# Performance work log

Hardware: AMD Instinct MI355X
Metric: run time of the kernel (lower is better)

The kernel has to match this reference:

```python
import jax, jax.numpy as jnp
import numpy as np

# Qwen3-Next GatedDeltaNet dims (tp_size = 1)
H = 2048          # hidden_size
HK, HV = 16, 32   # num_k_heads, num_v_heads
G = HV // HK      # v-heads per k-head
DK, DV = 128, 128 # head_k_dim, head_v_dim
KEY_DIM = HK * DK        # 2048
VAL_DIM = HV * DV        # 4096
CONV_DIM = 2 * KEY_DIM + VAL_DIM   # 8192
QKVZ = 2 * KEY_DIM + 2 * VAL_DIM   # 12288
BA = 2 * HV
K = 4             # conv kernel size
L = 4096          # tokens (one prefill sequence)
EPS = 1e-6


def setup_inputs() -> dict:
    key = jax.random.key(0)
    ks = jax.random.split(key, 5)
    s = lambda k, shape, sc: jax.random.normal(k, shape, jnp.float32) * sc
    return {
        'hidden_states': s(ks[0], (L, H), 1.0),
        'in_proj_w': s(ks[1], (H, QKVZ + BA), H ** -0.5),
        'conv_w': s(ks[2], (CONV_DIM, K), 0.25),
        'A_log': jnp.zeros((HV,), jnp.float32),
        'dt_bias': jnp.ones((HV,), jnp.float32),
        'norm_w': jnp.ones((DV,), jnp.float32),
        'out_proj_w': s(ks[3], (VAL_DIM, H), VAL_DIM ** -0.5),
    }


def _l2norm(x):
    return x * jax.lax.rsqrt(jnp.sum(x * x, axis=-1, keepdims=True) + EPS)


def _gdn_forward(hidden_states, in_proj_w, conv_w, A_log, dt_bias, norm_w, out_proj_w):
    # in_proj -> split qkvz / ba, fix_query_key_value_ordering
    proj = hidden_states @ in_proj_w                       # [L, QKVZ+BA]
    qkvz, ba = proj[:, :QKVZ], proj[:, QKVZ:]
    qkvz = qkvz.reshape(L, HK, 2 * DK + 2 * G * DV)        # per-k-head layout
    q = qkvz[:, :, :DK]                                    # [L,HK,DK]
    k = qkvz[:, :, DK:2 * DK]                              # [L,HK,DK]
    v = qkvz[:, :, 2 * DK:2 * DK + G * DV].reshape(L, HV, DV)
    z = qkvz[:, :, 2 * DK + G * DV:].reshape(L, HV, DV)
    ba = ba.reshape(L, HK, 2 * G)
    b = ba[:, :, :G].reshape(L, HV)
    a = ba[:, :, G:].reshape(L, HV)

    # depthwise causal conv1d over time (kernel K, left pad K-1) + silu
    mixed_qkv = jnp.concatenate(
        [q.reshape(L, KEY_DIM), k.reshape(L, KEY_DIM), v.reshape(L, VAL_DIM)], axis=-1)
    xp = jnp.pad(mixed_qkv, ((K - 1, 0), (0, 0)))
    conv_out = sum(conv_w[:, j] * xp[j:j + L] for j in range(K))
    mixed_qkv = jax.nn.silu(conv_out)

    q = mixed_qkv[:, :KEY_DIM].reshape(L, HK, DK)
    k = mixed_qkv[:, KEY_DIM:2 * KEY_DIM].reshape(L, HK, DK)
    v = mixed_qkv[:, 2 * KEY_DIM:].reshape(L, HV, DV)

    # gating: beta = sigmoid(b); g = -exp(A_log) * softplus(a + dt_bias)
    beta = jax.nn.sigmoid(b)                               # [L,HV]
    g = -jnp.exp(A_log) * jax.nn.softplus(a + dt_bias)     # [L,HV] (log decay)

    # expand k-heads to v-heads, qk l2-norm, scale q
    q = jnp.repeat(q, G, axis=1)                           # [L,HV,DK]
    k = jnp.repeat(k, G, axis=1)
    q = _l2norm(q) * (DK ** -0.5)
    k = _l2norm(k)

    # gated delta rule recurrence over time (state S: [HV, DK, DV])
    def step(S, inp):
        q_t, k_t, v_t, g_t, b_t = inp
        S = S * jnp.exp(g_t)[:, None, None]
        delta = (v_t - jnp.einsum('hk,hkv->hv', k_t, S)) * b_t[:, None]
        S = S + jnp.einsum('hk,hv->hkv', k_t, delta)
        o = jnp.einsum('hk,hkv->hv', q_t, S)
        return S, o

    S0 = jnp.zeros((HV, DK, DV), jnp.float32)
    _, core = jax.lax.scan(step, S0, (q, k, v, g, beta))   # core: [L,HV,DV]

    # gated RMSNorm (norm before gate): RMSNorm(x)*w*silu(z)
    var = jnp.mean(core * core, axis=-1, keepdims=True)
    core = core * jax.lax.rsqrt(var + EPS) * norm_w
    core = core * jax.nn.silu(z)

    return core.reshape(L, VAL_DIM) @ out_proj_w           # [L, H]


def reference(hidden_states, in_proj_w, conv_w, A_log, dt_bias, norm_w, out_proj_w):
    return _gdn_forward(hidden_states, in_proj_w, conv_w, A_log, dt_bias, norm_w, out_proj_w)
```

## Files before the change

kernel.cpp:

```cpp
#include <hip/hip_runtime.h>
#include <hip/hip_bf16.h>

#define L_SEQ 4096
#define HDIM 2048
#define NPROJA 8256
#define NPACK 12352
#define WLD 12352
#define EPS_ 1e-6f

using bf16 = __hip_bfloat16;
typedef __attribute__((ext_vector_type(8))) short short8;
typedef __attribute__((ext_vector_type(4))) float f32x4;

__device__ __forceinline__ float b2f(bf16 x) { return __bfloat162float(x); }
__device__ __forceinline__ bf16 f2b(float x) { return __float2bfloat16(x); }
__device__ __forceinline__ unsigned short b2u(bf16 x) {
  union { bf16 b; unsigned short u; } c; c.b = x; return c.u;
}
__device__ __forceinline__ void* swz(void* base, int row, int rowbytes, int colbyte) {
  return (void*)((char*)base + row * rowbytes + (colbyte ^ ((row & 7) << 4)));
}
__device__ __forceinline__ const void* swzc(const void* base, int row, int rowbytes, int colbyte) {
  return (const void*)((const char*)base + row * rowbytes + (colbyte ^ ((row & 7) << 4)));
}
__device__ __forceinline__ void* swzk(void* base, int row, int colbyte) {
  return (void*)((char*)base + row * 128 + (colbyte ^ (((row >> 3) & 7) << 4)));
}
__device__ __forceinline__ const void* swzkc(const void* base, int row, int colbyte) {
  return (const void*)((const char*)base + row * 128 + (colbyte ^ (((row >> 3) & 7) << 4)));
}

__device__ __forceinline__ void async_copy16(const void* g, void* l) {
  __builtin_amdgcn_global_load_lds(
      (const __attribute__((address_space(1))) void*)g,
      (__attribute__((address_space(3))) void*)l, 16, 0, 0);
}

__global__ __launch_bounds__(256) void cvt_bf16(const float* __restrict__ in,
                                                bf16* __restrict__ outp) {
  int i = (blockIdx.x * 256 + threadIdx.x) * 4;
  float4 v = *(const float4*)&in[i];
  bf16 o4[4] = {f2b(v.x), f2b(v.y), f2b(v.z), f2b(v.w)};
  *(ushort4*)&outp[i] = *(ushort4*)o4;
}

template <int MODE>
__device__ __forceinline__ int pmap(int n) {
  if constexpr (MODE == 3) {
    if (n < 2048) return (n >> 7) * 768 + (n & 127);
    else if (n < 4096) { int m = n - 2048; return (m >> 7) * 768 + 128 + (m & 127); }
    else if (n < 8192) { int m = n - 4096; return (m >> 8) * 768 + 256 + (m & 255); }
    else if (n < 8256) return 12288 + (n - 8192);
    else { int m = n - 8256; return (m >> 8) * 768 + 512 + (m & 255); }
  } else {
    return n;
  }
}

template <int MODE>
__global__ __launch_bounds__(256) void transpose_w(
    const float* __restrict__ W, bf16* __restrict__ Bt, int ldw, int Kd) {
  __shared__ float T[64][65];
  const int nb = blockIdx.x * 64, kb = blockIdx.y * 64;
  const int tid = threadIdx.x;
  const int c = tid & 63, gq = tid >> 6;
  const int sbase = pmap<MODE>(nb);
#pragma unroll
  for (int i = 0; i < 16; ++i) {
    int r = gq * 16 + i;
    T[c][r] = W[(size_t)(kb + r) * ldw + sbase + c];
  }
  __syncthreads();
#pragma unroll
  for (int i = 0; i < 16; ++i) {
    int n = gq * 16 + i;
    Bt[(size_t)(nb + n) * Kd + kb + c] = f2b(T[n][c]);
  }
}

template <int ROUTE>
__global__ __launch_bounds__(256) void gemm_bt(
    const bf16* __restrict__ A, const bf16* __restrict__ Bt,
    void* __restrict__ Cp, bf16* __restrict__ Cz, int N, int Kd,
    int MBnum, int NBnum) {
  __shared__ bf16 As[2][128 * 32];
  __shared__ bf16 Bs[2][128 * 32];
  const int tid = threadIdx.x;
  const int wave = tid >> 6, lane = tid & 63;
  const int l15 = lane & 15, quad = lane >> 4;

  int m_blk, n_blk;
  {
    const int CW = 32;
    int fullc = NBnum / CW;
    int rem = NBnum - fullc * CW;
    int thr = fullc * CW * MBnum;
    int wg = blockIdx.x;
    if (wg < thr) {
      int cw = CW * MBnum;
      int chunk = wg / cw, w = wg - chunk * cw;
      n_blk = chunk * CW + (w & (CW - 1));
      m_blk = w / CW;
    } else {
      int w2 = wg - thr;
      int r = rem ? rem : 1;
      n_blk = fullc * CW + w2 % r;
      m_blk = w2 / r;
    }
  }
  const int m0 = m_blk * 128, n0 = n_blk * 128;
  const int mw = (wave >> 1) * 64, nw = (wave & 1) * 64;

  f32x4 acc[4][4];
#pragma unroll
  for (int i = 0; i < 4; i++)
#pragma unroll
    for (int j = 0; j < 4; j++) acc[i][j] = {0.f, 0.f, 0.f, 0.f};

  const bf16* a_src0 = A + (size_t)(m0 + (tid >> 2)) * Kd + (tid & 3) * 8;
  const bf16* a_src1 = a_src0 + (size_t)64 * Kd;
  const bf16* b_src0 = Bt + (size_t)(n0 + (tid >> 2)) * Kd + (tid & 3) * 8;
  const bf16* b_src1 = b_src0 + (size_t)64 * Kd;
  const int d0 = tid * 8, d1 = (tid + 256) * 8;

  async_copy16(a_src0, &As[0][d0]);
  async_copy16(a_src1, &As[0][d1]);
  async_copy16(b_src0, &Bs[0][d0]);
  async_copy16(b_src1, &Bs[0][d1]);

  int cur = 0;
  for (int k0 = 0; k0 < Kd; k0 += 32, cur ^= 1) {
    __syncthreads();
    if (k0 + 32 < Kd) {
      const int nk = k0 + 32, nb = cur ^ 1;
      async_copy16(a_src0 + nk, &As[nb][d0]);
      async_copy16(a_src1 + nk, &As[nb][d1]);
      async_copy16(b_src0 + nk, &Bs[nb][d0]);
      async_copy16(b_src1 + nk, &Bs[nb][d1]);
    }
    short8 af[4], bfr[4];
#pragma unroll
    for (int i = 0; i < 4; i++)
      af[i] = *(const short8*)&As[cur][(mw + i * 16 + l15) * 32 + quad * 8];
#pragma unroll
    for (int j = 0; j < 4; j++)
      bfr[j] = *(const short8*)&Bs[cur][(nw + j * 16 + l15) * 32 + quad * 8];
#pragma unroll
    for (int i = 0; i < 4; i++)
#pragma unroll
      for (int j = 0; j < 4; j++)
        acc[i][j] = __builtin_amdgcn_mfma_f32_16x16x32_bf16(af[i], bfr[j],
                                                            acc[i][j], 0, 0, 0);
  }

#pragma unroll
  for (int i = 0; i < 4; i++) {
#pragma unroll
    for (int j = 0; j < 4; j++) {
      int col = n0 + nw + j * 16 + l15;
      if (col < N) {
#pragma unroll
        for (int r = 0; r < 4; r++) {
          int row = m0 + mw + i * 16 + quad * 4 + r;
          if (ROUTE == 0) {
            ((float*)Cp)[(size_t)row * N + col] = acc[i][j][r];
          } else {
            if (col < NPROJA)
              ((bf16*)Cp)[(size_t)row * NPROJA + col] = f2b(acc[i][j][r]);
            else
              Cz[(size_t)row * 4096 + (col - NPROJA)] = f2b(acc[i][j][r]);
          }
        }
      }
    }
  }
}

__global__ __launch_bounds__(128) void conv_norm_qk(
    const bf16* __restrict__ proj, const float* __restrict__ conv_w,
    bf16* __restrict__ qn, bf16* __restrict__ kn) {
  const int t = blockIdx.x >> 4, hk = blockIdx.x & 15;
  const int d = threadIdx.x;
  const int cq = hk * 128 + d;
  const int ck = 2048 + hk * 128 + d;
  float sq = 0.f, sk = 0.f;
#pragma unroll
  for (int j = 0; j < 4; j++) {
    int ts = t + j - 3;
    if (ts >= 0) {
      sq += conv_w[cq * 4 + j] * b2f(proj[(size_t)ts * NPROJA + cq]);
      sk += conv_w[ck * 4 + j] * b2f(proj[(size_t)ts * NPROJA + ck]);
    }
  }
  float qv = sq / (1.f + expf(-sq));
  float kv = sk / (1.f + expf(-sk));
  float ssq = qv * qv, ssk = kv * kv;
#pragma unroll
  for (int off = 32; off > 0; off >>= 1) {
    ssq += __shfl_down(ssq, off, 64);
    ssk += __shfl_down(ssk, off, 64);
  }
  __shared__ float red[4];
  if ((d & 63) == 0) {
    red[(d >> 6) * 2] = ssq;
    red[(d >> 6) * 2 + 1] = ssk;
  }
  __syncthreads();
  float sumq = red[0] + red[2];
  float sumk = red[1] + red[3];
  size_t o = (size_t)(t * 16 + hk) * 128 + d;
  qn[o] = f2b(qv * rsqrtf(sumq + EPS_) * 0.08838834764831845f);
  kn[o] = f2b(kv * rsqrtf(sumk + EPS_));
}

__global__ __launch_bounds__(256) void conv_silu_v(
    const bf16* __restrict__ proj, const float* __restrict__ conv_w,
    bf16* __restrict__ vbuf) {
  int idx = blockIdx.x * 256 + threadIdx.x;
  int t = idx >> 12, c = idx & 4095;
  int chan = 4096 + c;
  float s = 0.f;
#pragma unroll
  for (int j = 0; j < 4; j++) {
    int ts = t + j - 3;
    if (ts >= 0) s += conv_w[chan * 4 + j] * b2f(proj[(size_t)ts * NPROJA + chan]);
  }
  vbuf[idx] = f2b(s / (1.f + expf(-s)));
}

__global__ __launch_bounds__(256) void compute_bg(
    const bf16* __restrict__ proj, const float* __restrict__ A_log,
    const float* __restrict__ dt_bias, float* __restrict__ beta_arr,
    float* __restrict__ g_arr) {
  int idx = blockIdx.x * 256 + threadIdx.x;
  int t = idx >> 5, hv = idx & 31;
  size_t base = (size_t)t * NPROJA + 8192 + (hv >> 1) * 4 + (hv & 1);
  float b = b2f(proj[base]);
  float a = b2f(proj[base + 2]);
  beta_arr[idx] = 1.f / (1.f + expf(-b));
  float x = a + dt_bias[hv];
  float sp = (x > 20.f) ? x : log1pf(expf(x));
  g_arr[idx] = -expf(A_log[hv]) * sp;
}

__global__ __launch_bounds__(512) void precompute_chunk(
    const bf16* __restrict__ kn, const bf16* __restrict__ vbuf,
    const float* __restrict__ g_arr, const float* __restrict__ beta_arr,
    bf16* __restrict__ TV, bf16* __restrict__ TK) {
  const int c = blockIdx.x >> 5, h = blockIdx.x & 31, hk = h >> 1;
  const int t0 = c * 64, tid = threadIdx.x;
  const int wave = tid >> 6, lane = tid & 63, l15 = lane & 15, quad = lane >> 4;
  __shared__ bf16 Ks[64 * 128];
  __shared__ float X[64][256];
  __shared__ float BA[64][65];
  __shared__ float cgs[64], bet[64], eKs[64];

  {
    const int row = tid >> 4, s = tid & 15;
    short8 v0 = *(const short8*)(kn + ((size_t)(t0 + row) * 16 + hk) * 128 + s * 8);
    short8 v1 = *(const short8*)(kn + ((size_t)(t0 + 32 + row) * 16 + hk) * 128 + s * 8);
    *(short8*)swz(Ks, row, 256, s * 16) = v0;
    *(short8*)swz(Ks, row + 32, 256, s * 16) = v1;
  }
  if (tid < 64) {
    float bb = beta_arr[(size_t)(t0 + tid) * 32 + h];
    bet[tid] = bb;
    float x = g_arr[(size_t)(t0 + tid) * 32 + h];
#pragma unroll
    for (int off = 1; off < 64; off <<= 1) {
      float o = __shfl_up(x, off, 64);
      if (tid >= off) x += o;
    }
    cgs[tid] = x;
    eKs[tid] = bb * expf(x);
  }
  __syncthreads();

#pragma unroll
  for (int s = 0; s < 2; ++s) {
    const int b = wave * 2 + s, bi = b >> 2, bj = b & 3;
    if (bi >= bj) {
      f32x4 acc = {0.f, 0.f, 0.f, 0.f};
      const int ar = bi * 16 + l15, br = bj * 16 + l15;
#pragma unroll
      for (int ks = 0; ks < 4; ++ks) {
        const int cb = ks * 64 + quad * 16;
        short8 af = *(const short8*)swzc(Ks, ar, 256, cb);
        short8 bf = *(const short8*)swzc(Ks, br, 256, cb);
        acc = __builtin_amdgcn_mfma_f32_16x16x32_bf16(af, bf, acc, 0, 0, 0);
      }
#pragma unroll
      for (int r = 0; r < 4; ++r) {
        const int i = bi * 16 + quad * 4 + r, j = bj * 16 + l15;
        if (j < i) BA[i][j] = bet[i] * expf(cgs[i] - cgs[j]) * acc[r];
      }
    }
  }
  {
    const int i = tid >> 4, s = tid & 15;
#pragma unroll
    for (int half = 0; half < 2; ++half) {
      const int row = i + half * 32;
      short8 vv = *(const short8*)(vbuf + (size_t)(t0 + row) * 4096 + h * 128 + s * 8);
      short8 kv = *(const short8*)swzc(Ks, row, 256, s * 16);
      bf16 tv_[8], tk_[8];
      *(short8*)tv_ = vv;
      *(short8*)tk_ = kv;
      const float bb = bet[row], ee = eKs[row];
      float o0[8], o1[8];
#pragma unroll
      for (int k = 0; k < 8; ++k) {
        o0[k] = bb * b2f(tv_[k]);
        o1[k] = ee * b2f(tk_[k]);
      }
      *(float4*)&X[row][s * 8] = *(float4*)&o0[0];
      *(float4*)&X[row][s * 8 + 4] = *(float4*)&o0[4];
      *(float4*)&X[row][128 + s * 8] = *(float4*)&o1[0];
      *(float4*)&X[row][128 + s * 8 + 4] = *(float4*)&o1[4];
    }
  }

  const int li = tid >> 5, g4 = (tid & 31) * 4;
#pragma unroll
  for (int t = 0; t < 4; ++t) {
    const int i0 = t * 16;
    __syncthreads();
    if (t > 0) {
      const int gi = i0 + li;
      float4 a0 = *(float4*)&X[gi][g4];
      float4 a1 = *(float4*)&X[gi][128 + g4];
      for (int j = 0; j < i0; ++j) {
        const float bij = BA[gi][j];
        float4 x0 = *(float4*)&X[j][g4];
        float4 x1 = *(float4*)&X[j][128 + g4];
        a0.x -= bij * x0.x; a0.y -= bij * x0.y;
        a0.z -= bij * x0.z; a0.w -= bij * x0.w;
        a1.x -= bij * x1.x; a1.y -= bij * x1.y;
        a1.z -= bij * x1.z; a1.w -= bij * x1.w;
      }
      *(float4*)&X[gi][g4] = a0;
      *(float4*)&X[gi][128 + g4] = a1;
      __syncthreads();
    }
    if (tid < 256) {
      const int d = tid;
#pragma unroll
      for (int i2 = 1; i2 < 16; ++i2) {
        const int i = i0 + i2;
        float s = 0.f;
        for (int j = i0; j < i; ++j) s += BA[i][j] * X[j][d];
        X[i][d] -= s;
      }
    }
  }
  __syncthreads();
  for (int e = tid; e < 8192; e += 512) {
    int i = e >> 7, d = e & 127;
    size_t o = ((size_t)(t0 + i) * 32 + h) * 128 + d;
    TV[o] = f2b(X[i][d]);
    TK[o] = f2b(X[i][128 + d]);
  }
}

__global__ __launch_bounds__(512) void seq_kernel(
    bf16* TVU,
    const bf16* __restrict__ TKg, const bf16* __restrict__ qn,
    const bf16* __restrict__ kn, const float* __restrict__ g_arr,
    bf16* __restrict__ Oin) {
  const int h = blockIdx.x >> 1, dvh = blockIdx.x & 1, hk = h >> 1;
  const int dv0 = dvh * 64;
  const int tid = threadIdx.x;
  const int wave = tid >> 6, lane = tid & 63, l15 = lane & 15, quad = lane >> 4;
  const int mi = wave >> 1, half = wave & 1;
  const int srow = tid >> 4, scol = tid & 15;

  __shared__ bf16 STh[64 * 128], STl[64 * 128];
  __shared__ bf16 UTh[64 * 64], UTl[64 * 64];
  __shared__ bf16 TKs[64 * 128];
  __shared__ bf16 Qts[64 * 128];
  __shared__ bf16 KhT[128 * 64];

  for (int e = tid; e < 4096; e += 512) {
    ((unsigned int*)STh)[e] = 0u;
    ((unsigned int*)STl)[e] = 0u;
  }
  f32x4 Sf[4];
#pragma unroll
  for (int i = 0; i < 4; i++) Sf[i] = {0.f, 0.f, 0.f, 0.f};

  short8 tkr0, tkr1, qr0, qr1, kr0, kr1;
  float gv;
  auto issue_loads = [&](int c) {
    const size_t t0 = (size_t)c << 6;
    tkr0 = *(const short8*)(TKg + ((t0 + srow) * 32 + h) * 128 + scol * 8);
    tkr1 = *(const short8*)(TKg + ((t0 + 32 + srow) * 32 + h) * 128 + scol * 8);
    qr0 = *(const short8*)(qn + ((t0 + srow) * 16 + hk) * 128 + scol * 8);
    qr1 = *(const short8*)(qn + ((t0 + 32 + srow) * 16 + hk) * 128 + scol * 8);
    kr0 = *(const short8*)(kn + ((t0 + srow) * 16 + hk) * 128 + scol * 8);
    kr1 = *(const short8*)(kn + ((t0 + 32 + srow) * 16 + hk) * 128 + scol * 8);
    gv = g_arr[(t0 + lane) * 32 + h];
  };
  issue_loads(0);

  for (int c = 0; c < 64; ++c) {
    const int t0 = c << 6;
    __syncthreads();

    bf16 tvp[2][4];
#pragma unroll
    for (int nj = 0; nj < 2; nj++) {
      const int nrow = half * 32 + nj * 16 + l15;
#pragma unroll
      for (int r = 0; r < 4; r++) {
        const int i = mi * 16 + quad * 4 + r;
        tvp[nj][r] = TVU[((size_t)(t0 + i) * 32 + h) * 128 + dv0 + nrow];
      }
    }
    float cg = gv;
#pragma unroll
    for (int off = 1; off < 64; off <<= 1) {
      float o = __shfl_up(cg, off, 64);
      if (lane >= off) cg += o;
    }
    const float cg63 = __shfl(cg, 63, 64);
    const float lam = expf(cg63);
    const float fq = expf(cg);
    const float fk = expf(cg63 - cg);
    *(short8*)swz(TKs, srow, 256, scol * 16) = tkr0;
    *(short8*)swz(TKs, srow + 32, 256, scol * 16) = tkr1;
    {
      const float f0 = __shfl(fq, srow, 64);
      const float f1 = __shfl(fq, srow + 32, 64);
      bf16 ta[8], tb[8];
      *(short8*)ta = qr0;
      *(short8*)tb = qr1;
#pragma unroll
      for (int k = 0; k < 8; k++) {
        ta[k] = f2b(b2f(ta[k]) * f0);
        tb[k] = f2b(b2f(tb[k]) * f1);
      }
      *(short8*)swz(Qts, srow, 256, scol * 16) = *(short8*)ta;
      *(short8*)swz(Qts, srow + 32, 256, scol * 16) = *(short8*)tb;
    }
    {
      const float f0 = __shfl(fk, srow, 64);
      const float f1 = __shfl(fk, srow + 32, 64);
      bf16 ka[8], kb[8];
      *(short8*)ka = kr0;
      *(short8*)kb = kr1;
#pragma unroll
      for (int k = 0; k < 8; k++) {
        const int dk = scol * 8 + k;
        *(bf16*)swzk(KhT, dk, srow * 2) = f2b(b2f(ka[k]) * f0);
        *(bf16*)swzk(KhT, dk, (srow + 32) * 2) = f2b(b2f(kb[k]) * f1);
      }
    }
    issue_loads(c + 1 < 64 ? c + 1 : 63);
    __syncthreads();

    f32x4 oacc[2], xacc[2];
#pragma unroll
    for (int nj = 0; nj < 2; nj++) { oacc[nj] = {0.f,0.f,0.f,0.f}; xacc[nj] = {0.f,0.f,0.f,0.f}; }
    const int arow = mi * 16 + l15;
#pragma unroll
    for (int ks = 0; ks < 4; ++ks) {
      const int cb = ks * 64 + quad * 16;
      short8 aq = *(const short8*)swzc(Qts, arow, 256, cb);
      short8 at = *(const short8*)swzc(TKs, arow, 256, cb);
#pragma unroll
      for (int nj = 0; nj < 2; nj++) {
        const int nrow = half * 32 + nj * 16 + l15;
        short8 bh = *(const short8*)swzc(STh, nrow, 256, cb);
        short8 bl = *(const short8*)swzc(STl, nrow, 256, cb);
        oacc[nj] = __builtin_amdgcn_mfma_f32_16x16x32_bf16(aq, bh, oacc[nj], 0, 0, 0);
        xacc[nj] = __builtin_amdgcn_mfma_f32_16x16x32_bf16(at, bh, xacc[nj], 0, 0, 0);
        xacc[nj] = __builtin_amdgcn_mfma_f32_16x16x32_bf16(at, bl, xacc[nj], 0, 0, 0);
      }
    }
    const int krow = wave * 16 + l15;
    short8 ak0 = *(const short8*)swzkc(KhT, krow, 0 * 64 + quad * 16);
    short8 ak1 = *(const short8*)swzkc(KhT, krow, 1 * 64 + quad * 16);

#pragma unroll
    for (int nj = 0; nj < 2; nj++) {
      const int nrow = half * 32 + nj * 16 + l15;
      unsigned short ph[4], pl[4];
#pragma unroll
      for (int r = 0; r < 4; ++r) {
        const int i = mi * 16 + quad * 4 + r;
        const size_t go = ((size_t)(t0 + i) * 32 + h) * 128 + dv0 + nrow;
        Oin[go] = f2b(oacc[nj][r]);
        float uv = b2f(tvp[nj][r]) - xacc[nj][r];
        bf16 hb = f2b(uv);
        TVU[go] = hb;
        ph[r] = b2u(hb);
        pl[r] = b2u(f2b(uv - b2f(hb)));
      }
      const int cb = (mi * 16 + quad * 4) * 2;
      ushort4 vh; vh.x = ph[0]; vh.y = ph[1]; vh.z = ph[2]; vh.w = ph[3];
      ushort4 vl; vl.x = pl[0]; vl.y = pl[1]; vl.z = pl[2]; vl.w = pl[3];
      *(ushort4*)swz(UTh, nrow, 128, cb) = vh;
      *(ushort4*)swz(UTl, nrow, 128, cb) = vl;
    }
    __syncthreads();

#pragma unroll
    for (int nj = 0; nj < 4; nj++) {
      Sf[nj][0] *= lam; Sf[nj][1] *= lam; Sf[nj][2] *= lam; Sf[nj][3] *= lam;
    }
#pragma unroll
    for (int ks = 0; ks < 2; ++ks) {
      const short8 ak = ks ? ak1 : ak0;
      const int cb = ks * 64 + quad * 16;
#pragma unroll
      for (int nj = 0; nj < 4; nj++) {
        const int nrow = nj * 16 + l15;
        short8 bh = *(const short8*)swzc(UTh, nrow, 128, cb);
        short8 bl = *(const short8*)swzc(UTl, nrow, 128, cb);
        Sf[nj] = __builtin_amdgcn_mfma_f32_16x16x32_bf16(ak, bh, Sf[nj], 0, 0, 0);
        Sf[nj] = __builtin_amdgcn_mfma_f32_16x16x32_bf16(ak, bl, Sf[nj], 0, 0, 0);
      }
    }
#pragma unroll
    for (int nj = 0; nj < 4; nj++) {
      const int nrow = nj * 16 + l15;
      unsigned short ph[4], pl[4];
#pragma unroll
      for (int r = 0; r < 4; ++r) {
        float s = Sf[nj][r];
        bf16 hb = f2b(s);
        ph[r] = b2u(hb);
        pl[r] = b2u(f2b(s - b2f(hb)));
      }
      const int cb = (wave * 16 + quad * 4) * 2;
      ushort4 vh; vh.x = ph[0]; vh.y = ph[1]; vh.z = ph[2]; vh.w = ph[3];
      ushort4 vl; vl.x = pl[0]; vl.y = pl[1]; vl.z = pl[2]; vl.w = pl[3];
      *(ushort4*)swz(STh, nrow, 256, cb) = vh;
      *(ushort4*)swz(STl, nrow, 256, cb) = vl;
    }
  }
}

__global__ __launch_bounds__(512) void pass2_kernel(
    bf16* UC,
    const bf16* __restrict__ Oin, const bf16* __restrict__ qn,
    const bf16* __restrict__ kn, const float* __restrict__ g_arr,
    const bf16* __restrict__ zbuf, const float* __restrict__ norm_w) {
  const int c = blockIdx.x >> 5, h = blockIdx.x & 31, hk = h >> 1;
  const int t0 = c * 64, tid = threadIdx.x;
  __shared__ float Qf[64][129], Kf[64][129];
  __shared__ float Uf[64][128];
  __shared__ float Of[64][129];
  __shared__ float At[64][65];
  __shared__ float cgs[64], nw[128];

  for (int e = tid; e < 1024; e += 512) {
    int row = e >> 4, s = e & 15;
    size_t qko = ((size_t)(t0 + row) * 16 + hk) * 128 + s * 8;
    size_t uo = ((size_t)(t0 + row) * 32 + h) * 128 + s * 8;
    short8 vq = *(const short8*)(qn + qko);
    short8 vk = *(const short8*)(kn + qko);
    short8 vu = *(const short8*)(UC + uo);
    short8 vo = *(const short8*)(Oin + uo);
    bf16 tq[8], tk[8], tu[8], to[8];
    *(short8*)tq = vq; *(short8*)tk = vk; *(short8*)tu = vu; *(short8*)to = vo;
#pragma unroll
    for (int k = 0; k < 8; ++k) {
      Qf[row][s * 8 + k] = b2f(tq[k]);
      Kf[row][s * 8 + k] = b2f(tk[k]);
      Uf[row][s * 8 + k] = b2f(tu[k]);
      Of[row][s * 8 + k] = b2f(to[k]);
    }
  }
  if (tid < 64) {
    float x = g_arr[(size_t)(t0 + tid) * 32 + h];
#pragma unroll
    for (int off = 1; off < 64; off <<= 1) {
      float o = __shfl_up(x, off, 64);
      if (tid >= off) x += o;
    }
    cgs[tid] = x;
  }
  if (tid < 128) nw[tid] = norm_w[tid];
  __syncthreads();
  {
    const int ti = tid >> 4, tj = tid & 15;
    float acc[2][4];
#pragma unroll
    for (int r = 0; r < 2; ++r)
#pragma unroll
      for (int s = 0; s < 4; ++s) acc[r][s] = 0.f;
    for (int dk = 0; dk < 128; ++dk) {
      float a0 = Qf[ti * 2 + 0][dk], a1 = Qf[ti * 2 + 1][dk];
      float c0 = Kf[tj * 4 + 0][dk], c1 = Kf[tj * 4 + 1][dk];
      float c2 = Kf[tj * 4 + 2][dk], c3 = Kf[tj * 4 + 3][dk];
      acc[0][0] += a0 * c0; acc[0][1] += a0 * c1; acc[0][2] += a0 * c2; acc[0][3] += a0 * c3;
      acc[1][0] += a1 * c0; acc[1][1] += a1 * c1; acc[1][2] += a1 * c2; acc[1][3] += a1 * c3;
    }
#pragma unroll
    for (int r = 0; r < 2; ++r)
#pragma unroll
      for (int s = 0; s < 4; ++s) {
        int i = ti * 2 + r, j = tj * 4 + s;
        At[i][j] = (j <= i) ? expf(cgs[i] - cgs[j]) * acc[r][s] : 0.f;
      }
  }
  __syncthreads();
  {
    const int ri = tid >> 4, tn = tid & 15;
    float acc[2][8];
#pragma unroll
    for (int r = 0; r < 2; ++r)
#pragma unroll
      for (int k = 0; k < 8; ++k) acc[r][k] = 0.f;
    for (int j = 0; j < 64; ++j) {
      float a0 = At[ri * 2 + 0][j], a1 = At[ri * 2 + 1][j];
#pragma unroll
      for (int k = 0; k < 8; ++k) {
        float u = Uf[j][tn + 16 * k];
        acc[0][k] += a0 * u;
        acc[1][k] += a1 * u;
      }
    }
#pragma unroll
    for (int r = 0; r < 2; ++r)
#pragma unroll
      for (int k = 0; k < 8; ++k)
        Of[ri * 2 + r][tn + 16 * k] += acc[r][k];
  }
  __syncthreads();
  {
    const int r = tid >> 3, q8 = tid & 7;
    float ss = 0.f;
#pragma unroll
    for (int k = 0; k < 16; ++k) {
      float v = Of[r][q8 + 8 * k];
      ss += v * v;
    }
    ss += __shfl_xor(ss, 1, 64);
    ss += __shfl_xor(ss, 2, 64);
    ss += __shfl_xor(ss, 4, 64);
    float scale = rsqrtf(ss * (1.f / 128.f) + EPS_);
#pragma unroll
    for (int k = 0; k < 16; ++k) {
      int n = q8 + 8 * k;
      float val = Of[r][n] * scale * nw[n];
      float zz = b2f(zbuf[(size_t)(t0 + r) * 4096 + h * 128 + n]);
      val *= zz / (1.f + expf(-zz));
      UC[((size_t)(t0 + r) * 32 + h) * 128 + n] = f2b(val);
    }
  }
}

extern "C" void kernel_launch(void* const* d_in, const int* in_sizes, int n_in,
                              void* d_out, int out_size, void* d_ws,
                              size_t ws_size, hipStream_t stream) {
  const float* hidden = (const float*)d_in[0];
  const float* in_w = (const float*)d_in[1];
  const float* conv_w = (const float*)d_in[2];
  const float* A_log = (const float*)d_in[3];
  const float* dt_bias = (const float*)d_in[4];
  const float* norm_w = (const float*)d_in[5];
  const float* out_w = (const float*)d_in[6];
  float* out = (float*)d_out;

  char* p = (char*)d_ws;
  bf16* projA = (bf16*)p;
  bf16* TV = (bf16*)p;
  bf16* TK = (bf16*)(p + 33554432ULL);
  bf16* zbuf = (bf16*)(p + 67633152ULL);
  char* pR = p + 101187584ULL;
  bf16* vbuf = (bf16*)pR;
  float* beta = (float*)(pR + 33554432ULL);
  float* g = (float*)(pR + 34078720ULL);
  bf16* qn = (bf16*)(pR + 34603008ULL);
  bf16* kn = (bf16*)(pR + 51380224ULL);
  bf16* Bt_in = (bf16*)pR;
  bf16* hb16 = (bf16*)(pR + 50659328ULL);
  bf16* Bt_out = (bf16*)zbuf;

  cvt_bf16<<<(L_SEQ * HDIM) / 1024, 256, 0, stream>>>(hidden, hb16);
  transpose_w<3><<<dim3(193, 32), 256, 0, stream>>>(in_w, Bt_in, WLD, HDIM);
  gemm_bt<1><<<97 * 32, 256, 0, stream>>>(hb16, Bt_in, projA, zbuf,
                                          NPACK, HDIM, 32, 97);
  conv_norm_qk<<<L_SEQ * 16, 128, 0, stream>>>(projA, conv_w, qn, kn);
  conv_silu_v<<<(L_SEQ * 4096) / 256, 256, 0, stream>>>(projA, conv_w, vbuf);
  compute_bg<<<(L_SEQ * 32) / 256, 256, 0, stream>>>(projA, A_log, dt_bias,
                                                     beta, g);
  precompute_chunk<<<2048, 512, 0, stream>>>(kn, vbuf, g, beta, TV, TK);
  seq_kernel<<<64, 512, 0, stream>>>(TV, TK, qn, kn, g, vbuf);
  pass2_kernel<<<2048, 512, 0, stream>>>(TV, vbuf, qn, kn, g, zbuf, norm_w);
  transpose_w<0><<<dim3(32, 64), 256, 0, stream>>>(out_w, Bt_out, 2048, 4096);
  gemm_bt<0><<<16 * 32, 256, 0, stream>>>(TV, Bt_out, out, nullptr,
                                          2048, 4096, 32, 16);
}
```

Before: 1.170 ms.

## Triple-buffer GEMM LDS pipeline and vectorize conv kernels to 8 channels per thread

The bf16 GEMM moves from double to triple buffering. Each k-step waits with vmcnt(4), so one tile load stays in flight while MFMAs run, and there is a single barrier per step. Separately, the conv+silu+l2norm kernel for q/k and the conv+silu kernel for v now give each thread 8 channels, using 16-byte loads and stores, float4 conv weights and a 16-lane xor-shuffle reduction instead of shared memory. This cuts launch count, memory transactions and sync overhead in the elementwise stages, at the cost of more LDS per GEMM block (which may lower occupancy) and more registers per thread.

```diff
diff --git a/kernel.cpp b/kernel.cpp
--- a/kernel.cpp
+++ b/kernel.cpp
@@ -83,8 +83,8 @@
     const bf16* __restrict__ A, const bf16* __restrict__ Bt,
     void* __restrict__ Cp, bf16* __restrict__ Cz, int N, int Kd,
     int MBnum, int NBnum) {
-  __shared__ bf16 As[2][128 * 32];
-  __shared__ bf16 Bs[2][128 * 32];
+  __shared__ bf16 As[3][128 * 32];
+  __shared__ bf16 Bs[3][128 * 32];
   const int tid = threadIdx.x;
   const int wave = tid >> 6, lane = tid & 63;
   const int l15 = lane & 15, quad = lane >> 4;
@@ -127,31 +127,47 @@
   async_copy16(a_src1, &As[0][d1]);
   async_copy16(b_src0, &Bs[0][d0]);
   async_copy16(b_src1, &Bs[0][d1]);
+  async_copy16(a_src0 + 32, &As[1][d0]);
+  async_copy16(a_src1 + 32, &As[1][d1]);
+  async_copy16(b_src0 + 32, &Bs[1][d0]);
+  async_copy16(b_src1 + 32, &Bs[1][d1]);
+
+  auto mfma_step = [&](int bsel) {
+    short8 af[4], bfr[4];
+#pragma unroll
+    for (int i = 0; i < 4; i++)
+      af[i] = *(const short8*)&As[bsel][(mw + i * 16 + l15) * 32 + quad * 8];
+#pragma unroll
+    for (int j = 0; j < 4; j++)
+      bfr[j] = *(const short8*)&Bs[bsel][(nw + j * 16 + l15) * 32 + quad * 8];
+#pragma unroll
+    for (int i = 0; i < 4; i++)
+#pragma unroll
+      for (int j = 0; j < 4; j++)
+        acc[i][j] = __builtin_amdgcn_mfma_f32_16x16x32_bf16(af[i], bfr[j],
+                                                            acc[i][j], 0, 0, 0);
+  };
 
   int cur = 0;
-  for (int k0 = 0; k0 < Kd; k0 += 32, cur ^= 1) {
-    __syncthreads();
-    if (k0 + 32 < Kd) {
-      const int nk = k0 + 32, nb = cur ^ 1;
+  for (int k0 = 0; k0 < Kd - 32; k0 += 32) {
+    asm volatile("s_waitcnt vmcnt(4)" ::: "memory");
+    __builtin_amdgcn_s_barrier();
+    __builtin_amdgcn_sched_barrier(0);
+    const int nk = k0 + 64;
+    if (nk < Kd) {
+      int nb = cur + 2; if (nb >= 3) nb -= 3;
       async_copy16(a_src0 + nk, &As[nb][d0]);
       async_copy16(a_src1 + nk, &As[nb][d1]);
       async_copy16(b_src0 + nk, &Bs[nb][d0]);
       async_copy16(b_src1 + nk, &Bs[nb][d1]);
     }
-    short8 af[4], bfr[4];
-#pragma unroll
-    for (int i = 0; i < 4; i++)
-      af[i] = *(const short8*)&As[cur][(mw + i * 16 + l15) * 32 + quad * 8];
-#pragma unroll
-    for (int j = 0; j < 4; j++)
-      bfr[j] = *(const short8*)&Bs[cur][(nw + j * 16 + l15) * 32 + quad * 8];
-#pragma unroll
-    for (int i = 0; i < 4; i++)
-#pragma unroll
-      for (int j = 0; j < 4; j++)
-        acc[i][j] = __builtin_amdgcn_mfma_f32_16x16x32_bf16(af[i], bfr[j],
-                                                            acc[i][j], 0, 0, 0);
-  }
+    mfma_step(cur);
+    cur = (cur + 1 == 3) ? 0 : cur + 1;
+  }
+  asm volatile("s_waitcnt vmcnt(0)" ::: "memory");
+  __builtin_amdgcn_s_barrier();
+  __builtin_amdgcn_sched_barrier(0);
+  mfma_step(cur);
 
 #pragma unroll
   for (int i = 0; i < 4; i++) {
@@ -179,53 +195,90 @@
 __global__ __launch_bounds__(128) void conv_norm_qk(
     const bf16* __restrict__ proj, const float* __restrict__ conv_w,
     bf16* __restrict__ qn, bf16* __restrict__ kn) {
-  const int t = blockIdx.x >> 4, hk = blockIdx.x & 15;
-  const int d = threadIdx.x;
-  const int cq = hk * 128 + d;
-  const int ck = 2048 + hk * 128 + d;
-  float sq = 0.f, sk = 0.f;
+  const int t = blockIdx.x >> 1, g = blockIdx.x & 1;
+  const int r = threadIdx.x >> 4, s = threadIdx.x & 15;
+  const int hk = g * 8 + r;
+  const int cq = hk * 128 + s * 8;
+  const int ck = 2048 + cq;
+  float4 cwq[8], cwk[8];
+#pragma unroll
+  for (int e = 0; e < 8; ++e) {
+    cwq[e] = *(const float4*)&conv_w[(cq + e) * 4];
+    cwk[e] = *(const float4*)&conv_w[(ck + e) * 4];
+  }
+  float aq[8], ak[8];
+#pragma unroll
+  for (int e = 0; e < 8; ++e) { aq[e] = 0.f; ak[e] = 0.f; }
 #pragma unroll
   for (int j = 0; j < 4; j++) {
     int ts = t + j - 3;
     if (ts >= 0) {
-      sq += conv_w[cq * 4 + j] * b2f(proj[(size_t)ts * NPROJA + cq]);
-      sk += conv_w[ck * 4 + j] * b2f(proj[(size_t)ts * NPROJA + ck]);
-    }
-  }
-  float qv = sq / (1.f + expf(-sq));
-  float kv = sk / (1.f + expf(-sk));
-  float ssq = qv * qv, ssk = kv * kv;
-#pragma unroll
-  for (int off = 32; off > 0; off >>= 1) {
-    ssq += __shfl_down(ssq, off, 64);
-    ssk += __shfl_down(ssk, off, 64);
-  }
-  __shared__ float red[4];
-  if ((d & 63) == 0) {
-    red[(d >> 6) * 2] = ssq;
-    red[(d >> 6) * 2 + 1] = ssk;
-  }
-  __syncthreads();
-  float sumq = red[0] + red[2];
-  float sumk = red[1] + red[3];
-  size_t o = (size_t)(t * 16 + hk) * 128 + d;
-  qn[o] = f2b(qv * rsqrtf(sumq + EPS_) * 0.08838834764831845f);
-  kn[o] = f2b(kv * rsqrtf(sumk + EPS_));
+      short8 vq = *(const short8*)(proj + (size_t)ts * NPROJA + cq);
+      short8 vk = *(const short8*)(proj + (size_t)ts * NPROJA + ck);
+      bf16 tq[8], tk[8];
+      *(short8*)tq = vq;
+      *(short8*)tk = vk;
+#pragma unroll
+      for (int e = 0; e < 8; ++e) {
+        aq[e] += ((const float*)&cwq[e])[j] * b2f(tq[e]);
+        ak[e] += ((const float*)&cwk[e])[j] * b2f(tk[e]);
+      }
+    }
+  }
+  float fq[8], fk[8], ssq = 0.f, ssk = 0.f;
+#pragma unroll
+  for (int e = 0; e < 8; ++e) {
+    fq[e] = aq[e] / (1.f + expf(-aq[e]));
+    fk[e] = ak[e] / (1.f + expf(-ak[e]));
+    ssq += fq[e] * fq[e];
+    ssk += fk[e] * fk[e];
+  }
+#pragma unroll
+  for (int off = 1; off < 16; off <<= 1) {
+    ssq += __shfl_xor(ssq, off, 64);
+    ssk += __shfl_xor(ssk, off, 64);
+  }
+  const float rq = rsqrtf(ssq + EPS_) * 0.08838834764831845f;
+  const float rk = rsqrtf(ssk + EPS_);
+  bf16 wq[8], wk[8];
+#pragma unroll
+  for (int e = 0; e < 8; ++e) {
+    wq[e] = f2b(fq[e] * rq);
+    wk[e] = f2b(fk[e] * rk);
+  }
+  size_t o = (size_t)(t * 16 + hk) * 128 + s * 8;
+  *(short8*)(qn + o) = *(short8*)wq;
+  *(short8*)(kn + o) = *(short8*)wk;
 }
 
 __global__ __launch_bounds__(256) void conv_silu_v(
     const bf16* __restrict__ proj, const float* __restrict__ conv_w,
     bf16* __restrict__ vbuf) {
   int idx = blockIdx.x * 256 + threadIdx.x;
-  int t = idx >> 12, c = idx & 4095;
-  int chan = 4096 + c;
-  float s = 0.f;
+  int t = idx >> 9, c8 = (idx & 511) * 8;
+  int chan = 4096 + c8;
+  float4 cw[8];
+#pragma unroll
+  for (int e = 0; e < 8; ++e) cw[e] = *(const float4*)&conv_w[(chan + e) * 4];
+  float acc[8];
+#pragma unroll
+  for (int e = 0; e < 8; ++e) acc[e] = 0.f;
 #pragma unroll
   for (int j = 0; j < 4; j++) {
     int ts = t + j - 3;
-    if (ts >= 0) s += conv_w[chan * 4 + j] * b2f(proj[(size_t)ts * NPROJA + chan]);
-  }
-  vbuf[idx] = f2b(s / (1.f + expf(-s)));
+    if (ts >= 0) {
+      short8 v = *(const short8*)(proj + (size_t)ts * NPROJA + chan);
+      bf16 tv[8];
+      *(short8*)tv = v;
+#pragma unroll
+      for (int e = 0; e < 8; ++e)
+        acc[e] += ((const float*)&cw[e])[j] * b2f(tv[e]);
+    }
+  }
+  bf16 o[8];
+#pragma unroll
+  for (int e = 0; e < 8; ++e) o[e] = f2b(acc[e] / (1.f + expf(-acc[e])));
+  *(short8*)(vbuf + (size_t)t * 4096 + c8) = *(short8*)o;
 }
 
 __global__ __launch_bounds__(256) void compute_bg(
@@ -683,8 +736,8 @@
   transpose_w<3><<<dim3(193, 32), 256, 0, stream>>>(in_w, Bt_in, WLD, HDIM);
   gemm_bt<1><<<97 * 32, 256, 0, stream>>>(hb16, Bt_in, projA, zbuf,
                                           NPACK, HDIM, 32, 97);
-  conv_norm_qk<<<L_SEQ * 16, 128, 0, stream>>>(projA, conv_w, qn, kn);
-  conv_silu_v<<<(L_SEQ * 4096) / 256, 256, 0, stream>>>(projA, conv_w, vbuf);
+  conv_norm_qk<<<L_SEQ * 2, 128, 0, stream>>>(projA, conv_w, qn, kn);
+  conv_silu_v<<<(L_SEQ * 512) / 256, 256, 0, stream>>>(projA, conv_w, vbuf);
   compute_bg<<<(L_SEQ * 32) / 256, 256, 0, stream>>>(projA, A_log, dt_bias,
                                                      beta, g);
   precompute_chunk<<<2048, 512, 0, stream>>>(kn, vbuf, g, beta, TV, TK);
```

Result: no change. 1.163 ms (-0.6%).
